# Performance work log

Measured on AMD Instinct MI355X. Metric: run time of the kernel, lower is better.

## Reference

```python
import jax, jax.numpy as jnp
import numpy as np

N_NODES = 100000
N_EDGES = 3200000
IN_CH = 16
HIDDEN = 32
NUM_HH = 1000


def setup_inputs() -> dict:
    key = jax.random.key(0)
    ks = jax.random.split(key, 10)
    x = jax.random.normal(ks[0], (N_NODES, IN_CH), dtype=jnp.float32)
    edge_index = jax.random.randint(ks[1], (2, N_EDGES), 0, N_NODES, dtype=jnp.int64)
    s = 1.0 / np.sqrt(IN_CH)
    w1_l = jax.random.uniform(ks[2], (IN_CH, HIDDEN), jnp.float32, -s, s)
    w1_r = jax.random.uniform(ks[3], (IN_CH, HIDDEN), jnp.float32, -s, s)
    b1 = jnp.zeros((HIDDEN,), jnp.float32)
    s2 = 1.0 / np.sqrt(HIDDEN)
    w2_l = jax.random.uniform(ks[4], (HIDDEN, HIDDEN), jnp.float32, -s2, s2)
    w2_r = jax.random.uniform(ks[5], (HIDDEN, HIDDEN), jnp.float32, -s2, s2)
    b2 = jnp.zeros((HIDDEN,), jnp.float32)
    fc_w = jax.random.uniform(ks[6], (HIDDEN, NUM_HH), jnp.float32, -s2, s2)
    fc_b = jnp.zeros((NUM_HH,), jnp.float32)
    return {"x": x, "edge_index": edge_index, "w1_l": w1_l, "w1_r": w1_r, "b1": b1,
            "w2_l": w2_l, "w2_r": w2_r, "b2": b2, "fc_w": fc_w, "fc_b": fc_b}


def _sage_conv(h, src, dst, w_l, w_r, b, n_nodes):
    # mean-aggregate source features onto targets (PyG SAGEConv, aggr='mean')
    msg = h[src]                                            # [E, F] gather
    agg = jax.ops.segment_sum(msg, dst, num_segments=n_nodes)
    cnt = jax.ops.segment_sum(jnp.ones((src.shape[0], 1), h.dtype), dst,
                              num_segments=n_nodes)
    mean = agg / jnp.maximum(cnt, 1.0)
    # out = lin_l(mean_neighbors) + lin_r(x); bias lives in lin_l
    return mean @ w_l + b + h @ w_r


def reference(x, edge_index, w1_l, w1_r, b1, w2_l, w2_r, b2, fc_w, fc_b):
    src, dst = edge_index[0], edge_index[1]
    n = x.shape[0]
    h = jax.nn.relu(_sage_conv(x, src, dst, w1_l, w1_r, b1, n))
    h = jax.nn.relu(_sage_conv(h, src, dst, w2_l, w2_r, b2, n))
    return h @ fc_w + fc_b
```

## Files before the change

### kernel.cpp

```cpp
#include <hip/hip_runtime.h>

#define N_NODES 100000
#define IN_CH 16
#define HIDDEN 32
#define NUM_HH 1000

#define NPB 128
#define NBUCK ((N_NODES + NPB - 1) / NPB)
#define NCHUNK 512
#define SCAN_N (NBUCK * NCHUNK)
#define S1_BLOCKS ((SCAN_N + 1023) / 1024)
#define SORT_CAP 6144

__global__ __launch_bounds__(256) void passA_count(const int* __restrict__ dst,
                                                   int* __restrict__ counts,
                                                   int n_edges, int cepb) {
  __shared__ int hist[NBUCK];
  for (int i = threadIdx.x; i < NBUCK; i += 256) hist[i] = 0;
  __syncthreads();
  const int s = blockIdx.x * cepb;
  const int e = min(n_edges, s + cepb);
  for (int i = s + threadIdx.x; i < e; i += 256)
    atomicAdd(&hist[dst[i] >> 7], 1);
  __syncthreads();
  for (int i = threadIdx.x; i < NBUCK; i += 256)
    counts[i * NCHUNK + blockIdx.x] = hist[i];
}

__global__ __launch_bounds__(1024) void scan_local(const int* __restrict__ in,
                                                   int* __restrict__ out,
                                                   int* __restrict__ partials) {
  __shared__ int tmp[1024];
  const int i = blockIdx.x * 1024 + threadIdx.x;
  const int v = (i < SCAN_N) ? in[i] : 0;
  tmp[threadIdx.x] = v;
  __syncthreads();
  for (int off = 1; off < 1024; off <<= 1) {
    int t = (threadIdx.x >= off) ? tmp[threadIdx.x - off] : 0;
    __syncthreads();
    tmp[threadIdx.x] += t;
    __syncthreads();
  }
  if (i < SCAN_N) out[i] = tmp[threadIdx.x] - v;
  if (threadIdx.x == 1023) partials[blockIdx.x] = tmp[threadIdx.x];
}

__global__ __launch_bounds__(512) void scan_partials(int* __restrict__ partials) {
  __shared__ int tmp[512];
  const int v = (threadIdx.x < S1_BLOCKS) ? partials[threadIdx.x] : 0;
  tmp[threadIdx.x] = v;
  __syncthreads();
  for (int off = 1; off < 512; off <<= 1) {
    int t = (threadIdx.x >= off) ? tmp[threadIdx.x - off] : 0;
    __syncthreads();
    tmp[threadIdx.x] += t;
    __syncthreads();
  }
  if (threadIdx.x < S1_BLOCKS) partials[threadIdx.x] = tmp[threadIdx.x] - v;
}

__global__ __launch_bounds__(1024) void scan_add(int* __restrict__ out,
                                                 const int* __restrict__ partials,
                                                 int* __restrict__ bucket_ptr,
                                                 int n_edges) {
  const int i = blockIdx.x * 1024 + threadIdx.x;
  if (i < SCAN_N) {
    const int v = out[i] + partials[blockIdx.x];
    out[i] = v;
    if ((i & (NCHUNK - 1)) == 0) bucket_ptr[i / NCHUNK] = v;
  }
  if (i == 0) bucket_ptr[NBUCK] = n_edges;
}

__global__ __launch_bounds__(256) void passB_scatter(
    const int* __restrict__ src, const int* __restrict__ dst,
    const int* __restrict__ offs, unsigned* __restrict__ packed, int n_edges,
    int cepb) {
  __shared__ int cur[NBUCK];
  for (int i = threadIdx.x; i < NBUCK; i += 256)
    cur[i] = offs[i * NCHUNK + blockIdx.x];
  __syncthreads();
  const int s = blockIdx.x * cepb;
  const int e = min(n_edges, s + cepb);
  for (int i = s + threadIdx.x; i < e; i += 256) {
    const int d = dst[i];
    const int b = d >> 7;
    const int pos = atomicAdd(&cur[b], 1);
    packed[pos] = (unsigned)src[i] | ((unsigned)(d & (NPB - 1)) << 17);
  }
}

__global__ __launch_bounds__(512) void bucket_sort(
    unsigned* __restrict__ packed, const int* __restrict__ bucket_ptr,
    int* __restrict__ row_ptr, int n_edges) {
  __shared__ unsigned stage[SORT_CAP];
  __shared__ int bins[NPB];
  __shared__ int scn[NPB];
  __shared__ int cur[NPB];
  const int b = blockIdx.x;
  const int s = bucket_ptr[b];
  const int cnt = bucket_ptr[b + 1] - s;
  const int tid = threadIdx.x;

  if (tid < NPB) bins[tid] = 0;
  __syncthreads();
  for (int i = tid; i < cnt; i += 512) {
    const unsigned pk = packed[s + i];
    stage[i] = pk;
    atomicAdd(&bins[pk >> 17], 1);
  }
  __syncthreads();
  if (tid < NPB) scn[tid] = bins[tid];
  __syncthreads();
  for (int off = 1; off < NPB; off <<= 1) {
    int t = (tid < NPB && tid >= off) ? scn[tid - off] : 0;
    __syncthreads();
    if (tid < NPB) scn[tid] += t;
    __syncthreads();
  }
  if (tid < NPB) {
    const int excl = scn[tid] - bins[tid];
    cur[tid] = excl;
    const int node = b * NPB + tid;
    if (node < N_NODES) row_ptr[node] = s + excl;
  }
  if (b == NBUCK - 1 && tid == 0) row_ptr[N_NODES] = n_edges;
  __syncthreads();
  for (int i = tid; i < cnt; i += 512) {
    const unsigned pk = stage[i];
    const int pos = atomicAdd(&cur[pk >> 17], 1);
    packed[s + pos] = pk & 0x1FFFFu;
  }
}

template <int CH>
__global__ __launch_bounds__(256) void sage_fused(
    const float* __restrict__ feat, const int* __restrict__ row_ptr,
    const int* __restrict__ adj, const float* __restrict__ w_l,
    const float* __restrict__ w_r, const float* __restrict__ b,
    float* __restrict__ out) {
  constexpr int Q = CH / 4;
  constexpr int EPW = 64 / Q;
  __shared__ float wl[CH * HIDDEN];
  __shared__ float wr[CH * HIDDEN];
  __shared__ float bs[HIDDEN];
  __shared__ float mean_s[4][CH];
  __shared__ float xs[4][CH];
  for (int i = threadIdx.x; i < CH * HIDDEN; i += 256) {
    wl[i] = w_l[i];
    wr[i] = w_r[i];
  }
  if (threadIdx.x < HIDDEN) bs[threadIdx.x] = b[threadIdx.x];

  const int wave = threadIdx.x >> 6;
  const int lane = threadIdx.x & 63;
  const int n = blockIdx.x * 4 + wave;

  const int s = row_ptr[n];
  const int e = row_ptr[n + 1];
  const int q = lane % Q;
  const int esub = lane / Q;

  float4 acc = {0.f, 0.f, 0.f, 0.f};
  for (int i = s + esub; i < e; i += EPW) {
    const float4 v = ((const float4*)(feat + (size_t)adj[i] * CH))[q];
    acc.x += v.x;
    acc.y += v.y;
    acc.z += v.z;
    acc.w += v.w;
  }
#pragma unroll
  for (int m = Q; m < 64; m <<= 1) {
    acc.x += __shfl_xor(acc.x, m, 64);
    acc.y += __shfl_xor(acc.y, m, 64);
    acc.z += __shfl_xor(acc.z, m, 64);
    acc.w += __shfl_xor(acc.w, m, 64);
  }
  const float inv = 1.0f / fmaxf((float)(e - s), 1.0f);
  if (esub == 0) {
    mean_s[wave][4 * q + 0] = acc.x * inv;
    mean_s[wave][4 * q + 1] = acc.y * inv;
    mean_s[wave][4 * q + 2] = acc.z * inv;
    mean_s[wave][4 * q + 3] = acc.w * inv;
    const float4 xv = ((const float4*)(feat + (size_t)n * CH))[q];
    xs[wave][4 * q + 0] = xv.x;
    xs[wave][4 * q + 1] = xv.y;
    xs[wave][4 * q + 2] = xv.z;
    xs[wave][4 * q + 3] = xv.w;
  }
  __syncthreads();

  const int j = lane & 31;
  const int p = lane >> 5;
  float o = 0.f;
#pragma unroll
  for (int k = p * (CH / 2); k < (p + 1) * (CH / 2); ++k)
    o = fmaf(mean_s[wave][k], wl[k * HIDDEN + j],
             fmaf(xs[wave][k], wr[k * HIDDEN + j], o));
  o += __shfl_xor(o, 32, 64);
  if (p == 0) out[(size_t)n * HIDDEN + j] = fmaxf(o + bs[j], 0.f);
}

#define FC_BN 128
__global__ __launch_bounds__(256) void fc_kernel(
    const float* __restrict__ h, const float* __restrict__ fcw,
    const float* __restrict__ fcb, float* __restrict__ out) {
  __shared__ float hs[FC_BN * HIDDEN];
  int base = blockIdx.x * FC_BN;
  int nvalid = min(FC_BN, N_NODES - base);

  int cnt4 = nvalid * HIDDEN / 4;
  const float4* s4 = (const float4*)(h + (size_t)base * HIDDEN);
  for (int i = threadIdx.x; i < cnt4; i += 256) ((float4*)hs)[i] = s4[i];
  __syncthreads();

#pragma unroll
  for (int c = 0; c < 4; ++c) {
    int j = c * 256 + threadIdx.x;
    if (j < NUM_HH) {
      float w[HIDDEN];
#pragma unroll
      for (int k = 0; k < HIDDEN; ++k) w[k] = fcw[k * NUM_HH + j];
      float bias = fcb[j];
      int n = 0;
      for (; n + 2 <= nvalid; n += 2) {
        float a0 = bias, a1 = bias;
#pragma unroll
        for (int k = 0; k < HIDDEN; ++k) {
          a0 = fmaf(hs[n * HIDDEN + k], w[k], a0);
          a1 = fmaf(hs[(n + 1) * HIDDEN + k], w[k], a1);
        }
        out[(size_t)(base + n) * NUM_HH + j] = a0;
        out[(size_t)(base + n + 1) * NUM_HH + j] = a1;
      }
      for (; n < nvalid; ++n) {
        float a0 = bias;
#pragma unroll
        for (int k = 0; k < HIDDEN; ++k)
          a0 = fmaf(hs[n * HIDDEN + k], w[k], a0);
        out[(size_t)(base + n) * NUM_HH + j] = a0;
      }
    }
  }
}

extern "C" void kernel_launch(void* const* d_in, const int* in_sizes, int n_in,
                              void* d_out, int out_size, void* d_ws,
                              size_t ws_size, hipStream_t stream) {
  const float* x = (const float*)d_in[0];
  const int* edge = (const int*)d_in[1];
  const float* w1_l = (const float*)d_in[2];
  const float* w1_r = (const float*)d_in[3];
  const float* b1 = (const float*)d_in[4];
  const float* w2_l = (const float*)d_in[5];
  const float* w2_r = (const float*)d_in[6];
  const float* b2 = (const float*)d_in[7];
  const float* fc_w = (const float*)d_in[8];
  const float* fc_b = (const float*)d_in[9];
  float* out = (float*)d_out;

  const int n_edges = in_sizes[1] / 2;
  const int* src = edge;
  const int* dst = edge + n_edges;

  unsigned* packed = (unsigned*)d_ws;
  float* h1 = (float*)(packed + n_edges);
  float* h2 = h1 + (size_t)N_NODES * HIDDEN;
  int* counts = (int*)h2;
  int* offs = counts + SCAN_N;
  int* bucket_ptr = (int*)(h2 + (size_t)N_NODES * HIDDEN);
  int* partials = bucket_ptr + NBUCK + 1;
  int* row_ptr = partials + S1_BLOCKS + 1;

  const int cepb = (n_edges + NCHUNK - 1) / NCHUNK;
  const int sgrid = N_NODES / 4;
  const int fgrid = (N_NODES + FC_BN - 1) / FC_BN;

  passA_count<<<NCHUNK, 256, 0, stream>>>(dst, counts, n_edges, cepb);
  scan_local<<<S1_BLOCKS, 1024, 0, stream>>>(counts, offs, partials);
  scan_partials<<<1, 512, 0, stream>>>(partials);
  scan_add<<<S1_BLOCKS, 1024, 0, stream>>>(offs, partials, bucket_ptr, n_edges);
  passB_scatter<<<NCHUNK, 256, 0, stream>>>(src, dst, offs, packed, n_edges,
                                            cepb);
  bucket_sort<<<NBUCK, 512, 0, stream>>>(packed, bucket_ptr, row_ptr, n_edges);

  sage_fused<IN_CH><<<sgrid, 256, 0, stream>>>(x, row_ptr, (const int*)packed,
                                               w1_l, w1_r, b1, h1);
  sage_fused<HIDDEN><<<sgrid, 256, 0, stream>>>(h1, row_ptr, (const int*)packed,
                                                w2_l, w2_r, b2, h2);
  fc_kernel<<<fgrid, 256, 0, stream>>>(h2, fc_w, fc_b, out);
}
```

Baseline: 436.9 us.

## Fuse second SAGE layer with final FC and process 128 nodes per block

```diff
diff --git a/kernel.cpp b/kernel.cpp
--- a/kernel.cpp
+++ b/kernel.cpp
@@ -133,112 +133,110 @@
   }
 }
 
-template <int CH>
-__global__ __launch_bounds__(256) void sage_fused(
+template <int CH, bool FC>
+__global__ __launch_bounds__(512) void sage_block(
     const float* __restrict__ feat, const int* __restrict__ row_ptr,
     const int* __restrict__ adj, const float* __restrict__ w_l,
     const float* __restrict__ w_r, const float* __restrict__ b,
-    float* __restrict__ out) {
+    float* __restrict__ out, const float* __restrict__ fcw,
+    const float* __restrict__ fcb) {
   constexpr int Q = CH / 4;
   constexpr int EPW = 64 / Q;
   __shared__ float wl[CH * HIDDEN];
   __shared__ float wr[CH * HIDDEN];
   __shared__ float bs[HIDDEN];
-  __shared__ float mean_s[4][CH];
-  __shared__ float xs[4][CH];
-  for (int i = threadIdx.x; i < CH * HIDDEN; i += 256) {
+  __shared__ float mean_s[8][CH];
+  __shared__ float xs[8][CH];
+  __shared__ float hs[FC ? NPB * HIDDEN : 1];
+
+  const int tid = threadIdx.x;
+  for (int i = tid; i < CH * HIDDEN; i += 512) {
     wl[i] = w_l[i];
     wr[i] = w_r[i];
   }
-  if (threadIdx.x < HIDDEN) bs[threadIdx.x] = b[threadIdx.x];
-
-  const int wave = threadIdx.x >> 6;
-  const int lane = threadIdx.x & 63;
-  const int n = blockIdx.x * 4 + wave;
-
-  const int s = row_ptr[n];
-  const int e = row_ptr[n + 1];
-  const int q = lane % Q;
+  if (tid < HIDDEN) bs[tid] = b[tid];
+  __syncthreads();
+
+  const int wave = tid >> 6;
+  const int lane = tid & 63;
+  const int base = blockIdx.x * NPB;
+  const int q = lane & (Q - 1);
   const int esub = lane / Q;
-
-  float4 acc = {0.f, 0.f, 0.f, 0.f};
-  for (int i = s + esub; i < e; i += EPW) {
-    const float4 v = ((const float4*)(feat + (size_t)adj[i] * CH))[q];
-    acc.x += v.x;
-    acc.y += v.y;
-    acc.z += v.z;
-    acc.w += v.w;
-  }
-#pragma unroll
-  for (int m = Q; m < 64; m <<= 1) {
-    acc.x += __shfl_xor(acc.x, m, 64);
-    acc.y += __shfl_xor(acc.y, m, 64);
-    acc.z += __shfl_xor(acc.z, m, 64);
-    acc.w += __shfl_xor(acc.w, m, 64);
-  }
-  const float inv = 1.0f / fmaxf((float)(e - s), 1.0f);
-  if (esub == 0) {
-    mean_s[wave][4 * q + 0] = acc.x * inv;
-    mean_s[wave][4 * q + 1] = acc.y * inv;
-    mean_s[wave][4 * q + 2] = acc.z * inv;
-    mean_s[wave][4 * q + 3] = acc.w * inv;
-    const float4 xv = ((const float4*)(feat + (size_t)n * CH))[q];
-    xs[wave][4 * q + 0] = xv.x;
-    xs[wave][4 * q + 1] = xv.y;
-    xs[wave][4 * q + 2] = xv.z;
-    xs[wave][4 * q + 3] = xv.w;
-  }
-  __syncthreads();
-
   const int j = lane & 31;
   const int p = lane >> 5;
-  float o = 0.f;
-#pragma unroll
-  for (int k = p * (CH / 2); k < (p + 1) * (CH / 2); ++k)
-    o = fmaf(mean_s[wave][k], wl[k * HIDDEN + j],
-             fmaf(xs[wave][k], wr[k * HIDDEN + j], o));
-  o += __shfl_xor(o, 32, 64);
-  if (p == 0) out[(size_t)n * HIDDEN + j] = fmaxf(o + bs[j], 0.f);
-}
-
-#define FC_BN 128
-__global__ __launch_bounds__(256) void fc_kernel(
-    const float* __restrict__ h, const float* __restrict__ fcw,
-    const float* __restrict__ fcb, float* __restrict__ out) {
-  __shared__ float hs[FC_BN * HIDDEN];
-  int base = blockIdx.x * FC_BN;
-  int nvalid = min(FC_BN, N_NODES - base);
-
-  int cnt4 = nvalid * HIDDEN / 4;
-  const float4* s4 = (const float4*)(h + (size_t)base * HIDDEN);
-  for (int i = threadIdx.x; i < cnt4; i += 256) ((float4*)hs)[i] = s4[i];
-  __syncthreads();
-
-#pragma unroll
-  for (int c = 0; c < 4; ++c) {
-    int j = c * 256 + threadIdx.x;
-    if (j < NUM_HH) {
-      float w[HIDDEN];
-#pragma unroll
-      for (int k = 0; k < HIDDEN; ++k) w[k] = fcw[k * NUM_HH + j];
-      float bias = fcb[j];
-      int n = 0;
-      for (; n + 2 <= nvalid; n += 2) {
-        float a0 = bias, a1 = bias;
-#pragma unroll
-        for (int k = 0; k < HIDDEN; ++k) {
-          a0 = fmaf(hs[n * HIDDEN + k], w[k], a0);
-          a1 = fmaf(hs[(n + 1) * HIDDEN + k], w[k], a1);
+
+#pragma unroll 1
+  for (int pass = 0; pass < NPB / 8; ++pass) {
+    const int l = pass * 8 + wave;
+    const int n = base + l;
+    if (n < N_NODES) {
+      const int s = row_ptr[n];
+      const int e = row_ptr[n + 1];
+
+      float4 acc = {0.f, 0.f, 0.f, 0.f};
+      for (int i = s + esub; i < e; i += EPW) {
+        const float4 v = ((const float4*)(feat + (size_t)adj[i] * CH))[q];
+        acc.x += v.x;
+        acc.y += v.y;
+        acc.z += v.z;
+        acc.w += v.w;
+      }
+#pragma unroll
+      for (int m = Q; m < 64; m <<= 1) {
+        acc.x += __shfl_xor(acc.x, m, 64);
+        acc.y += __shfl_xor(acc.y, m, 64);
+        acc.z += __shfl_xor(acc.z, m, 64);
+        acc.w += __shfl_xor(acc.w, m, 64);
+      }
+      const float inv = 1.0f / fmaxf((float)(e - s), 1.0f);
+      if (esub == 0) {
+        mean_s[wave][4 * q + 0] = acc.x * inv;
+        mean_s[wave][4 * q + 1] = acc.y * inv;
+        mean_s[wave][4 * q + 2] = acc.z * inv;
+        mean_s[wave][4 * q + 3] = acc.w * inv;
+        const float4 xv = ((const float4*)(feat + (size_t)n * CH))[q];
+        xs[wave][4 * q + 0] = xv.x;
+        xs[wave][4 * q + 1] = xv.y;
+        xs[wave][4 * q + 2] = xv.z;
+        xs[wave][4 * q + 3] = xv.w;
+      }
+      __builtin_amdgcn_wave_barrier();
+
+      float o = 0.f;
+#pragma unroll
+      for (int k = p * (CH / 2); k < (p + 1) * (CH / 2); ++k)
+        o = fmaf(mean_s[wave][k], wl[k * HIDDEN + j],
+                 fmaf(xs[wave][k], wr[k * HIDDEN + j], o));
+      o += __shfl_xor(o, 32, 64);
+      o = fmaxf(o + bs[j], 0.f);
+      if (p == 0) {
+        if (FC)
+          hs[l * HIDDEN + j] = o;
+        else
+          out[(size_t)n * HIDDEN + j] = o;
+      }
+      __builtin_amdgcn_wave_barrier();
+    }
+  }
+
+  if (FC) {
+    __syncthreads();
+    const int nvalid = min(NPB, N_NODES - base);
+#pragma unroll
+    for (int c = 0; c < 2; ++c) {
+      const int jj = c * 512 + tid;
+      if (jj < NUM_HH) {
+        float w[HIDDEN];
+#pragma unroll
+        for (int k = 0; k < HIDDEN; ++k) w[k] = fcw[k * NUM_HH + jj];
+        const float bias = fcb[jj];
+        for (int n = 0; n < nvalid; ++n) {
+          float a = bias;
+#pragma unroll
+          for (int k = 0; k < HIDDEN; ++k)
+            a = fmaf(hs[n * HIDDEN + k], w[k], a);
+          out[(size_t)(base + n) * NUM_HH + jj] = a;
         }
-        out[(size_t)(base + n) * NUM_HH + j] = a0;
-        out[(size_t)(base + n + 1) * NUM_HH + j] = a1;
-      }
-      for (; n < nvalid; ++n) {
-        float a0 = bias;
-#pragma unroll
-        for (int k = 0; k < HIDDEN; ++k)
-          a0 = fmaf(hs[n * HIDDEN + k], w[k], a0);
-        out[(size_t)(base + n) * NUM_HH + j] = a0;
       }
     }
   }
@@ -265,16 +263,13 @@
 
   unsigned* packed = (unsigned*)d_ws;
   float* h1 = (float*)(packed + n_edges);
-  float* h2 = h1 + (size_t)N_NODES * HIDDEN;
-  int* counts = (int*)h2;
+  int* counts = (int*)(h1 + (size_t)N_NODES * HIDDEN);
   int* offs = counts + SCAN_N;
-  int* bucket_ptr = (int*)(h2 + (size_t)N_NODES * HIDDEN);
+  int* bucket_ptr = offs + SCAN_N;
   int* partials = bucket_ptr + NBUCK + 1;
   int* row_ptr = partials + S1_BLOCKS + 1;
 
   const int cepb = (n_edges + NCHUNK - 1) / NCHUNK;
-  const int sgrid = N_NODES / 4;
-  const int fgrid = (N_NODES + FC_BN - 1) / FC_BN;
 
   passA_count<<<NCHUNK, 256, 0, stream>>>(dst, counts, n_edges, cepb);
   scan_local<<<S1_BLOCKS, 1024, 0, stream>>>(counts, offs, partials);
@@ -284,9 +279,8 @@
                                             cepb);
   bucket_sort<<<NBUCK, 512, 0, stream>>>(packed, bucket_ptr, row_ptr, n_edges);
 
-  sage_fused<IN_CH><<<sgrid, 256, 0, stream>>>(x, row_ptr, (const int*)packed,
-                                               w1_l, w1_r, b1, h1);
-  sage_fused<HIDDEN><<<sgrid, 256, 0, stream>>>(h1, row_ptr, (const int*)packed,
-                                                w2_l, w2_r, b2, h2);
-  fc_kernel<<<fgrid, 256, 0, stream>>>(h2, fc_w, fc_b, out);
-}
+  sage_block<IN_CH, false><<<NBUCK, 512, 0, stream>>>(
+      x, row_ptr, (const int*)packed, w1_l, w1_r, b1, h1, nullptr, nullptr);
+  sage_block<HIDDEN, true><<<NBUCK, 512, 0, stream>>>(
+      h1, row_ptr, (const int*)packed, w2_l, w2_r, b2, out, fc_w, fc_b);
+}
```

Measured after the change: 459.5 us. +5.2%, slower.
